# Performance work log

Hardware: AMD Instinct MI355X
Metric: run time of the kernel (lower is better)

Reference implementation:

```python
import jax, jax.numpy as jnp
import numpy as np

SUB, E_NO, I_NO = 20, 2000, 500
T_DATA, T_SYN, T_HIST = 20000, 200, 50
SB, HB = 3, 3


def setup_inputs() -> dict:
    key = jax.random.key(0)
    ks = jax.random.split(key, 14)
    S_e = (jax.random.uniform(ks[0], (T_DATA, E_NO)) < 0.02).astype(jnp.float32)
    S_i = (jax.random.uniform(ks[1], (T_DATA, I_NO)) < 0.02).astype(jnp.float32)
    C_den = (jax.random.uniform(ks[2], (SUB, SUB)) < 0.1).astype(jnp.float32)
    C_syn_e = (jax.random.uniform(ks[3], (SUB, E_NO)) < 0.05).astype(jnp.float32)
    C_syn_i = (jax.random.uniform(ks[4], (SUB, I_NO)) < 0.05).astype(jnp.float32)
    W_syn = 0.1 * jax.random.normal(ks[5], (SUB, SB, 2))
    Tau_syn = jnp.tile(jnp.arange(SB, dtype=jnp.float32)[:, None], (1, 2))
    Delta_syn = jax.random.uniform(ks[6], (SUB, 2))
    W_hist = 0.1 * jax.random.normal(ks[7], (SUB, HB))
    Tau_hist = jnp.arange(HB, dtype=jnp.float32)
    Delta_hist = jax.random.uniform(ks[8], (SUB,))
    W_sub = jax.random.uniform(ks[9], (SUB,))
    V_o = jax.random.normal(ks[10], (1,))
    Theta = jnp.zeros((SUB,), jnp.float32)
    return {"S_e": S_e, "S_i": S_i, "C_den": C_den, "C_syn_e": C_syn_e,
            "C_syn_i": C_syn_i, "W_syn": W_syn, "Tau_syn": Tau_syn,
            "Delta_syn": Delta_syn, "W_hist": W_hist, "Tau_hist": Tau_hist,
            "Delta_hist": Delta_hist, "W_sub": W_sub, "V_o": V_o, "Theta": Theta}


def _alpha_kernels(delta, tau_log, W, T):
    # delta: [sub], tau_log: [B], W: [sub, B] -> kernels [sub, T]
    t = jnp.maximum(jnp.arange(T, dtype=jnp.float32)[None, :] - delta[:, None], 0.0)  # [sub,T]
    tt = t[:, None, :] / jnp.exp(tau_log)[None, :, None]  # [sub,B,T]
    return jnp.einsum('sbt,sb->st', tt * jnp.exp(-tt), W)


def _causal_conv(x, kern):
    # x: [T, sub], kern: [sub, T_k]; out[t,s] = sum_k kern[s,k] * x[t-k,s]
    Tk = kern.shape[1]
    xp = jnp.pad(x.T[None], ((0, 0), (0, 0), (Tk - 1, 0)))  # [1, sub, T+Tk-1]
    out = jax.lax.conv_general_dilated(
        xp, jnp.flip(kern, 1)[:, None, :], (1,), 'VALID',
        feature_group_count=kern.shape[0])
    return out[0].T  # [T, sub]


def reference(S_e, S_i, C_den, C_syn_e, C_syn_i, W_syn, Tau_syn, Delta_syn,
              W_hist, Tau_hist, Delta_hist, W_sub, V_o, Theta):
    # --- synaptic drive (vectorized over subunits) ---
    ke = _alpha_kernels(jnp.exp(Delta_syn[:, 0]), Tau_syn[:, 0], W_syn[:, :, 0], T_SYN)
    ki = _alpha_kernels(jnp.exp(Delta_syn[:, 1]), Tau_syn[:, 1], W_syn[:, :, 1], T_SYN)
    in_e = S_e @ C_syn_e.T  # [T, sub]
    in_i = S_i @ C_syn_i.T
    syn_in = _causal_conv(in_e, ke) + _causal_conv(in_i, ki)  # [T, sub]

    # --- history kernel ---
    hist_kern = _alpha_kernels(Delta_hist, Tau_hist, W_hist, T_HIST)  # [sub, T_hist]
    K = jnp.flip(hist_kern, 1)  # K[s, j] multiplies buffer entry j (oldest first)

    # --- sequential recurrence via scan ---
    def step(buf, syn_t):
        # buf: [T_hist, sub] = Y_pad[t : t+T_hist]
        h = jnp.einsum('js,sj->s', buf, K)
        prop = (buf[-1] * W_sub) @ C_den.T
        y = jnp.tanh(syn_t + prop + Theta + h)
        buf = jnp.concatenate([buf[1:], y[None]], 0)
        return buf, y

    buf0 = jnp.zeros((T_HIST, SUB), syn_in.dtype)
    _, Y = jax.lax.scan(step, buf0, syn_in)  # Y: [T, sub]
    return Y[:, 0] * W_sub[0] + V_o[0]
```

## Files before the change

kernel.cpp:

```cpp
#include <hip/hip_runtime.h>
#include <hip/hip_bf16.h>
#include <stdint.h>

#define SUBU 20
#define E_NO 2000
#define I_NO 500
#define T_DATA 20000
#define T_SYNK 200
#define T_HISTK 50
#define SBAS 3
#define HBAS 3
#define TPAD 20096
#define KSTORE 12

#define OFF_SYN  0
#define OFF_INE  401920
#define OFF_INI  803840
#define OFF_KE   1205760
#define OFF_KI   1209760
#define OFF_IIR  1213760
#define OFF_MW   1214760
#define OFF_MIDX 1215000
#define OFF_PAR  1215240
#define OFF_FLAG 1215264
#define OFF_Y    OFF_INI

#define TKC 2.8853900817779268f

__device__ __forceinline__ float bf2f(unsigned short u){
  unsigned v = ((unsigned)u) << 16; float f; __builtin_memcpy(&f, &v, 4); return f;
}
__device__ __forceinline__ float ldany(const void* p, int i, int bf){
  return bf ? bf2f(((const unsigned short*)p)[i]) : ((const float*)p)[i];
}

__global__ __launch_bounds__(256) void k_detect(const void* s_e, int* flag){
  __shared__ int found;
  if (threadIdx.x == 0) found = 0;
  __syncthreads();
  const unsigned* w = (const unsigned*)s_e;
  int hit = 0;
  for (int i = threadIdx.x; i < 8192; i += 256){
    unsigned x = w[i];
    if (x == 0x00003F80u || x == 0x3F803F80u) hit = 1;
  }
  if (hit) atomicOr(&found, 1);
  __syncthreads();
  if (threadIdx.x == 0) *flag = found;
}

__global__ __launch_bounds__(512) void k_prep(
    const void* Cden, const void* Wsyn, const void* Tausyn, const void* Dsyn,
    const void* Whist, const void* Tauhist, const void* Dhist,
    const void* Wsub, const void* Vo, const void* Theta, float* ws){
  int* wsi = (int*)ws;
  const int bf = wsi[OFF_FLAG];
  const int tx = threadIdx.x;
  __shared__ int mx;
  if (tx == 0) mx = 0;
  __syncthreads();
  for (int idx = tx; idx < SUBU * T_SYNK; idx += 512){
    int s = idx / T_SYNK, t = idx % T_SYNK;
    for (int c = 0; c < 2; ++c){
      float delta = __expf(ldany(Dsyn, s*2 + c, bf));
      float acc = 0.f;
      for (int b = 0; b < SBAS; ++b){
        float tau = __expf(ldany(Tausyn, b*2 + c, bf));
        float w   = ldany(Wsyn, (s*SBAS + b)*2 + c, bf);
        float tt  = fmaxf((float)t - delta, 0.f) / tau;
        acc += w * tt * __expf(-tt);
      }
      ws[(c == 0 ? OFF_KE : OFF_KI) + s*T_SYNK + t] = acc;
    }
  }
  if (tx < SUBU * HBAS){
    int s = tx / HBAS, b = tx % HBAS;
    float tau = __expf(ldany(Tauhist, b, bf));
    float w   = TKC * ldany(Whist, s*HBAS + b, bf);
    float dl  = ldany(Dhist, s, bf);
    float rho = __expf(-1.f / tau);
    float e1  = __expf(-(1.f - dl) / tau);
    float g1  = ((1.f - dl) / tau) * e1;
    float kap = rho / tau;
    float* c = ws + OFF_IIR + s*16 + b*4;
    c[0] = rho;
    c[1] = w * kap;
    c[2] = w * g1;
    c[3] = e1;
    if (b == 2){
      float e49 = __expf(-(49.f - dl) / tau);
      float g49 = ((49.f - dl) / tau) * e49;
      ws[OFF_IIR + s*16 + 12] = w * (rho*g49 + kap*e49);
      ws[OFF_IIR + s*16 + 13] = rho * e49;
    }
  }
  if (tx < SUBU){
    int s = tx, cnt = 0;
    float rowsum = 0.f;
    for (int sp = 0; sp < SUBU; ++sp){
      float c = ldany(Cden, s*SUBU + sp, bf);
      if (c != 0.f && cnt < KSTORE){
        float m = c * ldany(Wsub, sp, bf);
        rowsum += m;
        ws[OFF_MW + s*KSTORE + cnt]  = -2.f * TKC * m;
        wsi[OFF_MIDX + s*KSTORE + cnt] = sp;
        ++cnt;
      }
    }
    for (int k = cnt; k < KSTORE; ++k){
      ws[OFF_MW + s*KSTORE + k] = 0.f; wsi[OFF_MIDX + s*KSTORE + k] = 0;
    }
    atomicMax(&mx, cnt);
    ws[OFF_PAR + s] = TKC * (ldany(Theta, s, bf) + rowsum);
  }
  __syncthreads();
  if (tx == 0){
    ws[OFF_PAR + SUBU]     = ldany(Wsub, 0, bf);
    ws[OFF_PAR + SUBU + 1] = ldany(Vo, 0, bf);
    wsi[OFF_PAR + 23] = (mx <= 6) ? 6 : 12;
  }
}

template<int BF>
__device__ __forceinline__ void gemm_impl(const void* S, const void* C, int W,
                                          float* dst, int t0, int lane){
  float acc[4][SUBU];
  #pragma unroll
  for (int r = 0; r < 4; ++r)
    #pragma unroll
    for (int s = 0; s < SUBU; ++s) acc[r][s] = 0.f;
  for (int e = lane; e < W; e += 64){
    float s0 = ldany(S, (t0+0)*W + e, BF);
    float s1 = ldany(S, (t0+1)*W + e, BF);
    float s2 = ldany(S, (t0+2)*W + e, BF);
    float s3 = ldany(S, (t0+3)*W + e, BF);
    #pragma unroll
    for (int s = 0; s < SUBU; ++s){
      float c = ldany(C, s*W + e, BF);
      acc[0][s] = fmaf(s0, c, acc[0][s]);
      acc[1][s] = fmaf(s1, c, acc[1][s]);
      acc[2][s] = fmaf(s2, c, acc[2][s]);
      acc[3][s] = fmaf(s3, c, acc[3][s]);
    }
  }
  #pragma unroll
  for (int r = 0; r < 4; ++r){
    #pragma unroll
    for (int s = 0; s < SUBU; ++s){
      float v = acc[r][s];
      #pragma unroll
      for (int m = 32; m >= 1; m >>= 1) v += __shfl_xor(v, m, 64);
      if (lane == 0) dst[s*TPAD + t0 + r] = v;
    }
  }
}

__global__ __launch_bounds__(64) void k_gemm(const void* S, const void* C, int W,
                                             float* dst, const int* flagp){
  int t0 = blockIdx.x * 4, lane = threadIdx.x;
  if (*flagp) gemm_impl<1>(S, C, W, dst, t0, lane);
  else        gemm_impl<0>(S, C, W, dst, t0, lane);
}

__global__ __launch_bounds__(256) void k_conv(float* ws){
  const int s  = blockIdx.y;
  const int t0 = blockIdx.x * 256;
  const float* ine = ws + OFF_INE + s*TPAD;
  const float* ini = ws + OFF_INI + s*TPAD;
  __shared__ float eL[455], iL[455], keL[T_SYNK], kiL[T_SYNK];
  for (int j = threadIdx.x; j < 455; j += 256){
    int t = t0 - 199 + j;
    bool ok = (t >= 0 && t < TPAD);
    eL[j] = ok ? ine[t] : 0.f;
    iL[j] = ok ? ini[t] : 0.f;
  }
  for (int j = threadIdx.x; j < T_SYNK; j += 256){
    keL[j] = ws[OFF_KE + s*T_SYNK + j];
    kiL[j] = ws[OFF_KI + s*T_SYNK + j];
  }
  __syncthreads();
  int t = t0 + threadIdx.x;
  if (t < TPAD){
    float a0 = 0.f, a1 = 0.f;
    #pragma unroll 4
    for (int k = 0; k < T_SYNK; ++k){
      a0 = fmaf(keL[k], eL[threadIdx.x + 199 - k], a0);
      a1 = fmaf(kiL[k], iL[threadIdx.x + 199 - k], a1);
    }
    ws[OFF_SYN + s*TPAD + t] = fmaf(TKC, a0 + a1, ws[OFF_PAR + s]);
  }
}

__device__ __forceinline__ float get4(const float4& a, const float4& b,
                                      const float4& c, const float4& d, int u){
  const float4& q = (u < 4) ? a : ((u < 8) ? b : ((u < 12) ? c : d));
  int r = u & 3;
  return (r == 0) ? q.x : ((r == 1) ? q.y : ((r == 2) ? q.z : q.w));
}
__device__ __forceinline__ void set4(float4& a, float4& b, float4& c, float4& d,
                                     int u, float v){
  float4& q = (u < 4) ? a : ((u < 8) ? b : ((u < 12) ? c : d));
  int r = u & 3;
  if (r == 0) q.x = v; else if (r == 1) q.y = v; else if (r == 2) q.z = v; else q.w = v;
}

template<int KM, int BF>
__global__ __launch_bounds__(64, 1) void k_scan(float* ws, float* yout){
  const int* wsi = (const int*)ws;
  if ((wsi[OFF_FLAG] != 0) != (BF != 0)) return;
  if (wsi[OFF_PAR + 23] != KM) return;
  const int lane = threadIdx.x;
  const int s = lane < SUBU ? lane : SUBU - 1;
  float mwp[KM]; int mad[KM];
  #pragma unroll
  for (int k = 0; k < KM; ++k){
    mwp[k] = ws[OFF_MW + s*KSTORE + k];
    mad[k] = wsi[OFF_MIDX + s*KSTORE + k] * 4;
  }
  const float* cc = ws + OFF_IIR + s*16;
  const float rh0 = cc[0],  kp0 = cc[1],  ay0 = cc[2],  ey0 = cc[3];
  const float rh1 = cc[4],  kp1 = cc[5],  ay1 = cc[6],  ey1 = cc[7];
  const float rh2 = cc[8],  kp2 = cc[9],  ay2 = cc[10], ey2 = cc[11];
  const float cA  = cc[12], cE  = cc[13];
  const float wsub0 = ws[OFF_PAR + SUBU];
  const float vo    = ws[OFF_PAR + SUBU + 1];
  const float* syncol = ws + OFF_SYN + s*TPAD;

  float yhv[66];
  #pragma unroll
  for (int j = 0; j < 66; ++j) yhv[j] = 0.f;
  float A0 = 0.f, E0 = 0.f, A1 = 0.f, E1 = 0.f, A2 = 0.f, E2 = 0.f;
  float pb[KM];
  #pragma unroll
  for (int k = 0; k < KM; ++k) pb[k] = 0.5f;
  float4 u0 = *(const float4*)(syncol + 0);
  float4 u1 = *(const float4*)(syncol + 4);
  float4 u2 = *(const float4*)(syncol + 8);
  float4 u3 = *(const float4*)(syncol + 12);
  float4 n0, n1, n2, n3;
  float xpre = u0.x;

  auto block16 = [&](int tbase, float4& b0, float4& b1, float4& b2, float4& b3,
                     float4& p0, float4& p1, float4& p2, float4& p3){
    const float4* src = (const float4*)(syncol + tbase + 16);
    p0 = src[0]; p1 = src[1]; p2 = src[2]; p3 = src[3];
    float4 ob0, ob1, ob2, ob3;
    #pragma unroll
    for (int u = 0; u < 16; ++u){
      float acc0 = fmaf(mwp[0], pb[0], xpre);
      float acc1 = mwp[1] * pb[1];
      #pragma unroll
      for (int k = 2; k + 1 < KM; k += 2){
        acc0 = fmaf(mwp[k],   pb[k],   acc0);
        acc1 = fmaf(mwp[k+1], pb[k+1], acc1);
      }
      float X  = acc0 + acc1;
      float ex = __builtin_amdgcn_exp2f(X);
      float r  = __builtin_amdgcn_rcpf(ex + 1.f);
      int rb = __float_as_int(r);
      #pragma unroll
      for (int k = 0; k < KM; ++k)
        pb[k] = __int_as_float(__builtin_amdgcn_ds_bpermute(mad[k], rb));
      float y = fmaf(-2.f, r, 1.f);
      float yprev = yhv[u + 49];
      float yold  = yhv[u];
      float A0n = fmaf(rh0, A0, fmaf(kp0, E0, ay0 * yprev));
      E0 = fmaf(rh0, E0, ey0 * yprev); A0 = A0n;
      float A1n = fmaf(rh1, A1, fmaf(kp1, E1, ay1 * yprev));
      E1 = fmaf(rh1, E1, ey1 * yprev); A1 = A1n;
      float A2n = fmaf(rh2, A2, fmaf(kp2, E2, fmaf(-cA, yold, ay2 * yprev)));
      E2 = fmaf(rh2, E2, fmaf(-cE, yold, ey2 * yprev)); A2 = A2n;
      float h = (A0 + A1) + A2;
      float cn = (u < 15) ? get4(b0, b1, b2, b3, u + 1) : p0.x;
      xpre = cn + h;
      yhv[u + 50] = y;
      set4(ob0, ob1, ob2, ob3, u, fmaf(y, wsub0, vo));
    }
    #pragma unroll
    for (int j = 0; j < 50; ++j) yhv[j] = yhv[j + 16];
    if (lane == 0 && tbase + 16 <= T_DATA){
      float4* q = (float4*)(yout + tbase);
      q[0] = ob0; q[1] = ob1; q[2] = ob2; q[3] = ob3;
    }
  };

  #pragma unroll 1
  for (int ib = 0; ib < 628; ++ib){
    block16(ib*32,      u0, u1, u2, u3, n0, n1, n2, n3);
    block16(ib*32 + 16, n0, n1, n2, n3, u0, u1, u2, u3);
  }
}

__global__ __launch_bounds__(256) void k_out(const float* ws, void* outp){
  const int* wsi = (const int*)ws;
  if (wsi[OFF_FLAG] == 0) return;
  int i = blockIdx.x * 256 + threadIdx.x;
  if (i < T_DATA)
    ((__hip_bfloat16*)outp)[i] = __float2bfloat16(ws[OFF_Y + i]);
}

extern "C" void kernel_launch(void* const* d_in, const int* in_sizes, int n_in,
                              void* d_out, int out_size, void* d_ws, size_t ws_size,
                              hipStream_t stream){
  const void* S_e   = d_in[0];
  const void* S_i   = d_in[1];
  const void* C_den = d_in[2];
  const void* C_e   = d_in[3];
  const void* C_i   = d_in[4];
  const void* W_syn = d_in[5];
  const void* Tau_s = d_in[6];
  const void* D_syn = d_in[7];
  const void* W_hst = d_in[8];
  const void* Tau_h = d_in[9];
  const void* D_hst = d_in[10];
  const void* W_sub = d_in[11];
  const void* V_o   = d_in[12];
  const void* Theta = d_in[13];
  float* ws = (float*)d_ws;
  int* flagp = (int*)(ws + OFF_FLAG);

  k_detect<<<1, 256, 0, stream>>>(S_e, flagp);
  k_prep<<<1, 512, 0, stream>>>(C_den, W_syn, Tau_s, D_syn, W_hst, Tau_h, D_hst,
                                W_sub, V_o, Theta, ws);
  k_gemm<<<5000, 64, 0, stream>>>(S_e, C_e, E_NO, ws + OFF_INE, flagp);
  k_gemm<<<5000, 64, 0, stream>>>(S_i, C_i, I_NO, ws + OFF_INI, flagp);
  dim3 cgrid(79, 20);
  k_conv<<<cgrid, 256, 0, stream>>>(ws);
  k_scan<6, 0><<<1, 64, 0, stream>>>(ws, (float*)d_out);
  k_scan<6, 1><<<1, 64, 0, stream>>>(ws, ws + OFF_Y);
  k_scan<12, 0><<<1, 64, 0, stream>>>(ws, (float*)d_out);
  k_scan<12, 1><<<1, 64, 0, stream>>>(ws, ws + OFF_Y);
  k_out<<<79, 256, 0, stream>>>(ws, d_out);
}
```

Measured before the change: 2.160 ms.

## Two-step lookahead scan: compute neighbor activations locally to halve cross-lane permute latency

The sequential tanh recurrence now advances two timesteps per cross-lane exchange. Each lane speculatively recomputes the next-step activations of its dendritic neighbours, using second-order neighbour tables built in prep, so ds_bpermute round trips happen once per pair of steps instead of every step. Scan kernels are specialised on the maximum in-degree (3 to 6), with a 12-wide fallback. Output now always goes to the workspace and is copied out by k_out for both fp32 and bf16. This adds redundant exp/rcp work and more registers per lane, and the two-step path relies on a sparse connectivity matrix.

```diff
diff --git a/kernel.cpp b/kernel.cpp
--- a/kernel.cpp
+++ b/kernel.cpp
@@ -1,6 +1,7 @@
 #include <hip/hip_runtime.h>
 #include <hip/hip_bf16.h>
 #include <stdint.h>
+#include <type_traits>
 
 #define SUBU 20
 #define E_NO 2000
@@ -23,6 +24,8 @@
 #define OFF_MIDX 1215000
 #define OFF_PAR  1215240
 #define OFF_FLAG 1215264
+#define OFF_TAB  1215280
+#define TSTR     96
 #define OFF_Y    OFF_INI
 
 #define TKC 2.8853900817779268f
@@ -32,6 +35,11 @@
 }
 __device__ __forceinline__ float ldany(const void* p, int i, int bf){
   return bf ? bf2f(((const unsigned short*)p)[i]) : ((const float*)p)[i];
+}
+__device__ __forceinline__ float ex2(float x){ return __builtin_amdgcn_exp2f(x); }
+__device__ __forceinline__ float rcpa(float x){ return __builtin_amdgcn_rcpf(x); }
+__device__ __forceinline__ float bperm(int addr, float src){
+  return __int_as_float(__builtin_amdgcn_ds_bpermute(addr, __float_as_int(src)));
 }
 
 __global__ __launch_bounds__(256) void k_detect(const void* s_e, int* flag){
@@ -95,29 +103,54 @@
     }
   }
   if (tx < SUBU){
-    int s = tx, cnt = 0;
+    int s = tx, cntf = 0, cnt12 = 0;
     float rowsum = 0.f;
+    int idx6[6]; float w6[6];
     for (int sp = 0; sp < SUBU; ++sp){
       float c = ldany(Cden, s*SUBU + sp, bf);
-      if (c != 0.f && cnt < KSTORE){
+      if (c != 0.f){
         float m = c * ldany(Wsub, sp, bf);
         rowsum += m;
-        ws[OFF_MW + s*KSTORE + cnt]  = -2.f * TKC * m;
-        wsi[OFF_MIDX + s*KSTORE + cnt] = sp;
-        ++cnt;
+        if (cntf < 6){ idx6[cntf] = sp; w6[cntf] = -2.f * TKC * m; }
+        ++cntf;
+        if (cnt12 < KSTORE){
+          ws[OFF_MW + s*KSTORE + cnt12]  = -2.f * TKC * m;
+          wsi[OFF_MIDX + s*KSTORE + cnt12] = sp;
+          ++cnt12;
+        }
       }
     }
-    for (int k = cnt; k < KSTORE; ++k){
+    for (int k = cnt12; k < KSTORE; ++k){
       ws[OFF_MW + s*KSTORE + k] = 0.f; wsi[OFF_MIDX + s*KSTORE + k] = 0;
     }
-    atomicMax(&mx, cnt);
+    float* tb = ws + OFF_TAB + s*TSTR; int* tbi = (int*)tb;
+    for (int d = 0; d < 6; ++d){
+      bool v = (d < cntf) && (d < 6);
+      tb[d]     = v ? w6[d] : 0.f;
+      tbi[6+d]  = v ? idx6[d]*4 : 0;
+      int c2 = 0;
+      if (v){
+        int j = idx6[d];
+        for (int sp = 0; sp < SUBU && c2 < 6; ++sp){
+          float c = ldany(Cden, j*SUBU + sp, bf);
+          if (c != 0.f){
+            tb[12 + d*6 + c2]  = -2.f * TKC * c * ldany(Wsub, sp, bf);
+            tbi[48 + d*6 + c2] = sp*4;
+            ++c2;
+          }
+        }
+      }
+      for (int k = c2; k < 6; ++k){ tb[12+d*6+k] = 0.f; tbi[48+d*6+k] = 0; }
+    }
+    atomicMax(&mx, cntf);
     ws[OFF_PAR + s] = TKC * (ldany(Theta, s, bf) + rowsum);
   }
   __syncthreads();
   if (tx == 0){
     ws[OFF_PAR + SUBU]     = ldany(Wsub, 0, bf);
     ws[OFF_PAR + SUBU + 1] = ldany(Vo, 0, bf);
-    wsi[OFF_PAR + 23] = (mx <= 6) ? 6 : 12;
+    int D = mx;
+    wsi[OFF_PAR + 23] = (D <= 3) ? 3 : (D <= 6 ? D : 12);
   }
 }
 
@@ -191,6 +224,18 @@
   }
 }
 
+__device__ __forceinline__ float get9(const float4& a, const float4& b,
+                                      const float4& p, int i){
+  if (i >= 8) return p.x;
+  const float4& q = (i < 4) ? a : b;
+  int r = i & 3;
+  return (r == 0) ? q.x : ((r == 1) ? q.y : ((r == 2) ? q.z : q.w));
+}
+__device__ __forceinline__ void set8(float4& a, float4& b, int i, float v){
+  float4& q = (i < 4) ? a : b;
+  int r = i & 3;
+  if (r == 0) q.x = v; else if (r == 1) q.y = v; else if (r == 2) q.z = v; else q.w = v;
+}
 __device__ __forceinline__ float get4(const float4& a, const float4& b,
                                       const float4& c, const float4& d, int u){
   const float4& q = (u < 4) ? a : ((u < 8) ? b : ((u < 12) ? c : d));
@@ -204,19 +249,22 @@
   if (r == 0) q.x = v; else if (r == 1) q.y = v; else if (r == 2) q.z = v; else q.w = v;
 }
 
-template<int KM, int BF>
-__global__ __launch_bounds__(64, 1) void k_scan(float* ws, float* yout){
+template<int D>
+__global__ __launch_bounds__(64, 1) void k_scan2(float* ws, float* yout){
   const int* wsi = (const int*)ws;
-  if ((wsi[OFF_FLAG] != 0) != (BF != 0)) return;
-  if (wsi[OFF_PAR + 23] != KM) return;
+  if (wsi[OFF_PAR + 23] != D) return;
   const int lane = threadIdx.x;
   const int s = lane < SUBU ? lane : SUBU - 1;
-  float mwp[KM]; int mad[KM];
-  #pragma unroll
-  for (int k = 0; k < KM; ++k){
-    mwp[k] = ws[OFF_MW + s*KSTORE + k];
-    mad[k] = wsi[OFF_MIDX + s*KSTORE + k] * 4;
-  }
+  const float* tb = ws + OFF_TAB + s*TSTR;
+  const int* tbi = (const int*)tb;
+  float mwO[D]; int madO[D];
+  float mw2[D][D]; int mad2[D][D];
+  #pragma unroll
+  for (int d = 0; d < D; ++d){ mwO[d] = tb[d]; madO[d] = tbi[6+d]; }
+  #pragma unroll
+  for (int d = 0; d < D; ++d)
+    #pragma unroll
+    for (int k = 0; k < D; ++k){ mw2[d][k] = tb[12+d*6+k]; mad2[d][k] = tbi[48+d*6+k]; }
   const float* cc = ws + OFF_IIR + s*16;
   const float rh0 = cc[0],  kp0 = cc[1],  ay0 = cc[2],  ey0 = cc[3];
   const float rh1 = cc[4],  kp1 = cc[5],  ay1 = cc[6],  ey1 = cc[7];
@@ -226,10 +274,154 @@
   const float vo    = ws[OFF_PAR + SUBU + 1];
   const float* syncol = ws + OFF_SYN + s*TPAD;
 
+  constexpr int YHN = (D <= 4) ? 66 : 58;
+  float yhv[YHN];
+  #pragma unroll
+  for (int j = 0; j < YHN; ++j) yhv[j] = 0.f;
+  float A0=0.f,E0=0.f,A1=0.f,E1=0.f,A2=0.f,E2=0.f;
+  float rO[D], r2[D][D], Q[D];
+  #pragma unroll
+  for (int d = 0; d < D; ++d){
+    rO[d] = 0.5f;
+    #pragma unroll
+    for (int k = 0; k < D; ++k) r2[d][k] = 0.5f;
+  }
+  float4 u0 = *(const float4*)(syncol + 0);
+  float4 u1 = *(const float4*)(syncol + 4);
+  float4 n0, n1;
+  float xpreS = u0.x;
+  #pragma unroll
+  for (int d = 0; d < D; ++d) Q[d] = bperm(madO[d], xpreS);
+  int tbase = 0;
+
+  auto block8 = [&](auto OFS_, float4& c0, float4& c1, float4& p0, float4& p1){
+    constexpr int OFS = decltype(OFS_)::value;
+    const float4* src = (const float4*)(syncol + tbase + 8);
+    p0 = src[0]; p1 = src[1];
+    float4 ob0, ob1;
+    #pragma unroll
+    for (int u = 0; u < 4; ++u){
+      const int u2 = 2*u;
+      float ypm1 = yhv[OFS + u2 + 49];
+      float yo50 = yhv[OFS + u2];
+      float A0n = fmaf(rh0, A0, fmaf(kp0, E0, ay0 * ypm1));
+      E0 = fmaf(rh0, E0, ey0 * ypm1); A0 = A0n;
+      float A1n = fmaf(rh1, A1, fmaf(kp1, E1, ay1 * ypm1));
+      E1 = fmaf(rh1, E1, ey1 * ypm1); A1 = A1n;
+      float A2n = fmaf(rh2, A2, fmaf(kp2, E2, fmaf(-cA, yo50, ay2 * ypm1)));
+      E2 = fmaf(rh2, E2, fmaf(-cE, yo50, ey2 * ypm1)); A2 = A2n;
+      float xpre1 = get9(c0, c1, p0, u2 + 1) + ((A0 + A1) + A2);
+      float Xe;
+      { float a0 = fmaf(mwO[0], rO[0], xpreS), a1 = 0.f;
+        #pragma unroll
+        for (int k = 1; k < D; ++k){
+          if (k & 1) a1 = fmaf(mwO[k], rO[k], a1);
+          else       a0 = fmaf(mwO[k], rO[k], a0);
+        }
+        Xe = a0 + a1; }
+      float rE = rcpa(ex2(Xe) + 1.f);
+      float yE = fmaf(-2.f, rE, 1.f);
+      float rn[D];
+      #pragma unroll
+      for (int d = 0; d < D; ++d){
+        float a0 = fmaf(mw2[d][0], r2[d][0], Q[d]), a1 = 0.f;
+        #pragma unroll
+        for (int k = 1; k < D; ++k){
+          if (k & 1) a1 = fmaf(mw2[d][k], r2[d][k], a1);
+          else       a0 = fmaf(mw2[d][k], r2[d][k], a0);
+        }
+        rn[d] = rcpa(ex2(a0 + a1) + 1.f);
+      }
+      float Xo;
+      { float a0 = fmaf(mwO[0], rn[0], xpre1), a1 = 0.f;
+        #pragma unroll
+        for (int k = 1; k < D; ++k){
+          if (k & 1) a1 = fmaf(mwO[k], rn[k], a1);
+          else       a0 = fmaf(mwO[k], rn[k], a0);
+        }
+        Xo = a0 + a1; }
+      float rT1 = rcpa(ex2(Xo) + 1.f);
+      float yO = fmaf(-2.f, rT1, 1.f);
+      float yo49 = yhv[OFS + u2 + 1];
+      A0n = fmaf(rh0, A0, fmaf(kp0, E0, ay0 * yE));
+      E0 = fmaf(rh0, E0, ey0 * yE); A0 = A0n;
+      A1n = fmaf(rh1, A1, fmaf(kp1, E1, ay1 * yE));
+      E1 = fmaf(rh1, E1, ey1 * yE); A1 = A1n;
+      A2n = fmaf(rh2, A2, fmaf(kp2, E2, fmaf(-cA, yo49, ay2 * yE)));
+      E2 = fmaf(rh2, E2, fmaf(-cE, yo49, ey2 * yE)); A2 = A2n;
+      xpreS = get9(c0, c1, p0, u2 + 2) + ((A0 + A1) + A2);
+      int rb = __float_as_int(rT1);
+      #pragma unroll
+      for (int d = 0; d < D; ++d)
+        rO[d] = __int_as_float(__builtin_amdgcn_ds_bpermute(madO[d], rb));
+      #pragma unroll
+      for (int d = 0; d < D; ++d)
+        #pragma unroll
+        for (int k = 0; k < D; ++k)
+          r2[d][k] = __int_as_float(__builtin_amdgcn_ds_bpermute(mad2[d][k], rb));
+      int qb = __float_as_int(xpreS);
+      #pragma unroll
+      for (int d = 0; d < D; ++d)
+        Q[d] = __int_as_float(__builtin_amdgcn_ds_bpermute(madO[d], qb));
+      yhv[OFS + u2 + 50] = yE;
+      yhv[OFS + u2 + 51] = yO;
+      set8(ob0, ob1, u2,     fmaf(yE, wsub0, vo));
+      set8(ob0, ob1, u2 + 1, fmaf(yO, wsub0, vo));
+    }
+    if (lane == 0 && tbase + 8 <= T_DATA){
+      float4* q = (float4*)(yout + tbase);
+      q[0] = ob0; q[1] = ob1;
+    }
+    tbase += 8;
+  };
+
+  using IC0 = std::integral_constant<int,0>;
+  using IC8 = std::integral_constant<int,8>;
+  if constexpr (D <= 4){
+    #pragma unroll 1
+    for (int ib = 0; ib < 1256; ++ib){
+      block8(IC0{}, u0, u1, n0, n1);
+      block8(IC8{}, n0, n1, u0, u1);
+      #pragma unroll
+      for (int j = 0; j < 50; ++j) yhv[j] = yhv[j + 16];
+    }
+  } else {
+    #pragma unroll 1
+    for (int ib = 0; ib < 1256; ++ib){
+      block8(IC0{}, u0, u1, n0, n1);
+      #pragma unroll
+      for (int j = 0; j < 50; ++j) yhv[j] = yhv[j + 8];
+      block8(IC0{}, n0, n1, u0, u1);
+      #pragma unroll
+      for (int j = 0; j < 50; ++j) yhv[j] = yhv[j + 8];
+    }
+  }
+}
+
+__global__ __launch_bounds__(64, 1) void k_scanfb(float* ws, float* yout){
+  const int* wsi = (const int*)ws;
+  if (wsi[OFF_PAR + 23] != 12) return;
+  const int lane = threadIdx.x;
+  const int s = lane < SUBU ? lane : SUBU - 1;
+  constexpr int KM = 12;
+  float mwp[KM]; int mad[KM];
+  #pragma unroll
+  for (int k = 0; k < KM; ++k){
+    mwp[k] = ws[OFF_MW + s*KSTORE + k];
+    mad[k] = wsi[OFF_MIDX + s*KSTORE + k] * 4;
+  }
+  const float* cc = ws + OFF_IIR + s*16;
+  const float rh0 = cc[0],  kp0 = cc[1],  ay0 = cc[2],  ey0 = cc[3];
+  const float rh1 = cc[4],  kp1 = cc[5],  ay1 = cc[6],  ey1 = cc[7];
+  const float rh2 = cc[8],  kp2 = cc[9],  ay2 = cc[10], ey2 = cc[11];
+  const float cA  = cc[12], cE  = cc[13];
+  const float wsub0 = ws[OFF_PAR + SUBU];
+  const float vo    = ws[OFF_PAR + SUBU + 1];
+  const float* syncol = ws + OFF_SYN + s*TPAD;
   float yhv[66];
   #pragma unroll
   for (int j = 0; j < 66; ++j) yhv[j] = 0.f;
-  float A0 = 0.f, E0 = 0.f, A1 = 0.f, E1 = 0.f, A2 = 0.f, E2 = 0.f;
+  float A0=0.f,E0=0.f,A1=0.f,E1=0.f,A2=0.f,E2=0.f;
   float pb[KM];
   #pragma unroll
   for (int k = 0; k < KM; ++k) pb[k] = 0.5f;
@@ -239,7 +431,6 @@
   float4 u3 = *(const float4*)(syncol + 12);
   float4 n0, n1, n2, n3;
   float xpre = u0.x;
-
   auto block16 = [&](int tbase, float4& b0, float4& b1, float4& b2, float4& b3,
                      float4& p0, float4& p1, float4& p2, float4& p3){
     const float4* src = (const float4*)(syncol + tbase + 16);
@@ -255,8 +446,7 @@
         acc1 = fmaf(mwp[k+1], pb[k+1], acc1);
       }
       float X  = acc0 + acc1;
-      float ex = __builtin_amdgcn_exp2f(X);
-      float r  = __builtin_amdgcn_rcpf(ex + 1.f);
+      float r  = rcpa(ex2(X) + 1.f);
       int rb = __float_as_int(r);
       #pragma unroll
       for (int k = 0; k < KM; ++k)
@@ -283,7 +473,6 @@
       q[0] = ob0; q[1] = ob1; q[2] = ob2; q[3] = ob3;
     }
   };
-
   #pragma unroll 1
   for (int ib = 0; ib < 628; ++ib){
     block16(ib*32,      u0, u1, u2, u3, n0, n1, n2, n3);
@@ -293,10 +482,13 @@
 
 __global__ __launch_bounds__(256) void k_out(const float* ws, void* outp){
   const int* wsi = (const int*)ws;
-  if (wsi[OFF_FLAG] == 0) return;
+  const int bf = wsi[OFF_FLAG];
   int i = blockIdx.x * 256 + threadIdx.x;
-  if (i < T_DATA)
-    ((__hip_bfloat16*)outp)[i] = __float2bfloat16(ws[OFF_Y + i]);
+  if (i < T_DATA){
+    float v = ws[OFF_Y + i];
+    if (bf) ((__hip_bfloat16*)outp)[i] = __float2bfloat16(v);
+    else    ((float*)outp)[i] = v;
+  }
 }
 
 extern "C" void kernel_launch(void* const* d_in, const int* in_sizes, int n_in,
@@ -326,9 +518,11 @@
   k_gemm<<<5000, 64, 0, stream>>>(S_i, C_i, I_NO, ws + OFF_INI, flagp);
   dim3 cgrid(79, 20);
   k_conv<<<cgrid, 256, 0, stream>>>(ws);
-  k_scan<6, 0><<<1, 64, 0, stream>>>(ws, (float*)d_out);
-  k_scan<6, 1><<<1, 64, 0, stream>>>(ws, ws + OFF_Y);
-  k_scan<12, 0><<<1, 64, 0, stream>>>(ws, (float*)d_out);
-  k_scan<12, 1><<<1, 64, 0, stream>>>(ws, ws + OFF_Y);
+  float* yout = ws + OFF_Y;
+  k_scan2<3><<<1, 64, 0, stream>>>(ws, yout);
+  k_scan2<4><<<1, 64, 0, stream>>>(ws, yout);
+  k_scan2<5><<<1, 64, 0, stream>>>(ws, yout);
+  k_scan2<6><<<1, 64, 0, stream>>>(ws, yout);
+  k_scanfb<<<1, 64, 0, stream>>>(ws, yout);
   k_out<<<79, 256, 0, stream>>>(ws, d_out);
 }
```

Result: slower. 4.083 ms (+89.0%).
